# Performance work log

Measured on AMD Instinct MI355X. Metric: run time of the kernel, lower is better.

Reference implementation:

```python
import jax, jax.numpy as jnp
import numpy as np

B_SZ = 2
D_MODEL = 1024
H = 16
C = 8
BLK = 128
DK = 64
DV = 64
NCHUNK = 1024            # tokens per chunk (divisible by BLK)
T = C * (1 + NCHUNK)     # 8200: [g0, chunk0..., g1, chunk1..., ...]


def setup_inputs() -> dict:
    key = jax.random.key(0)
    k0, k1, k2, k3, k4 = jax.random.split(key, 5)
    s = 0.02
    x  = jax.random.normal(k0, (B_SZ, T, D_MODEL), dtype=jnp.float32)
    Wq = jax.random.normal(k1, (D_MODEL, H * DK), dtype=jnp.float32) * s
    Wk = jax.random.normal(k2, (D_MODEL, H * DK), dtype=jnp.float32) * s
    Wv = jax.random.normal(k3, (D_MODEL, H * DV), dtype=jnp.float32) * s
    Wo = jax.random.normal(k4, (H * DV, D_MODEL), dtype=jnp.float32) * s
    bo = jnp.zeros((D_MODEL,), dtype=jnp.float32)
    return {"x": x, "Wq": Wq, "Wk": Wk, "Wv": Wv, "Wo": Wo, "bo": bo}


def _local_sparse_3block(qf, kf, vf):
    # qf,kf: [BC, H, N, dk], vf: [BC, H, N, dv]; window = [left, current, right] blocks
    bc, h, n, dk = qf.shape
    dv = vf.shape[-1]
    nb = n // BLK
    q = qf.reshape(bc, h, nb, BLK, dk)
    k = kf.reshape(bc, h, nb, BLK, dk)
    v = vf.reshape(bc, h, nb, BLK, dv)
    zk = jnp.zeros((bc, h, 1, BLK, dk), qf.dtype)
    zv = jnp.zeros((bc, h, 1, BLK, dv), qf.dtype)
    kp = jnp.concatenate([zk, k, zk], axis=2)          # [bc,h,nb+2,B,dk]
    vp = jnp.concatenate([zv, v, zv], axis=2)
    k_win = jnp.concatenate([kp[:, :, 0:nb], kp[:, :, 1:nb + 1], kp[:, :, 2:nb + 2]], axis=3)  # [bc,h,nb,3B,dk]
    v_win = jnp.concatenate([vp[:, :, 0:nb], vp[:, :, 1:nb + 1], vp[:, :, 2:nb + 2]], axis=3)  # [bc,h,nb,3B,dv]
    scale = 1.0 / np.sqrt(dk).astype(np.float32)
    scores = jnp.einsum('bhnqd,bhnkd->bhnqk', q, k_win) * scale   # [bc,h,nb,B,3B]
    mask = np.zeros((nb, 3 * BLK), dtype=bool)
    mask[0, :BLK] = True           # first block: left padding invalid
    mask[-1, 2 * BLK:] = True      # last block: right padding invalid
    scores = jnp.where(jnp.asarray(mask)[None, None, :, None, :], -jnp.inf, scores)
    attn = jax.nn.softmax(scores, axis=-1)
    out = jnp.einsum('bhnqk,bhnkd->bhnqd', attn, v_win)
    return out.reshape(bc, h, n, dv)


def reference(x, Wq, Wk, Wv, Wo, bo):
    Bb, Tt, _ = x.shape
    q = (x @ Wq).reshape(Bb, Tt, H, DK).transpose(0, 2, 1, 3)  # [B,H,T,dk]
    k = (x @ Wk).reshape(Bb, Tt, H, DK).transpose(0, 2, 1, 3)
    v = (x @ Wv).reshape(Bb, Tt, H, DV).transpose(0, 2, 1, 3)
    stride = NCHUNK + 1
    g_idx = jnp.arange(C) * stride
    gq = q[:, :, g_idx]  # [B,H,C,dk]
    gk = k[:, :, g_idx]
    gv = v[:, :, g_idx]  # [B,H,C,dv]
    local_idx = ((g_idx + 1)[:, None] + jnp.arange(NCHUNK)[None, :]).reshape(-1)
    qx = q[:, :, local_idx].reshape(Bb, H, C, NCHUNK, DK)
    kx = k[:, :, local_idx].reshape(Bb, H, C, NCHUNK, DK)
    vx = v[:, :, local_idx].reshape(Bb, H, C, NCHUNK, DV)
    # local 3-block attention per chunk
    q_flat = qx.transpose(0, 2, 1, 3, 4).reshape(Bb * C, H, NCHUNK, DK)
    k_flat = kx.transpose(0, 2, 1, 3, 4).reshape(Bb * C, H, NCHUNK, DK)
    v_flat = vx.transpose(0, 2, 1, 3, 4).reshape(Bb * C, H, NCHUNK, DV)
    out_local = _local_sparse_3block(q_flat, k_flat, v_flat)
    out_local = out_local.reshape(Bb, C, H, NCHUNK, DV).transpose(0, 2, 1, 3, 4)  # [B,H,C,Nchunk,dv]
    # each local token additionally receives its chunk's global value directly
    out_chunks = out_local + gv[:, :, :, None, :]
    # global tokens attend over all globals + own chunk's locals (joint softmax, fp32)
    scale = 1.0 / np.sqrt(DK).astype(np.float32)
    scores_gg = jnp.einsum('bhcd,bhed->bhce', gq, gk) * scale      # [B,H,C,C]
    scores_gl = jnp.einsum('bhcd,bhcnd->bhcn', gq, kx) * scale     # [B,H,C,Nchunk]
    attn = jax.nn.softmax(jnp.concatenate([scores_gg, scores_gl], axis=-1), axis=-1)
    a_gg, a_gl = attn[..., :C], attn[..., C:]
    out_g = (jnp.einsum('bhce,bhed->bhcd', a_gg, gv)
             + jnp.einsum('bhcn,bhcnd->bhcd', a_gl, vx))           # [B,H,C,dv]
    out_inter = jnp.concatenate([out_g[:, :, :, None, :], out_chunks], axis=3)  # [B,H,C,1+Nchunk,dv]
    out = out_inter.reshape(Bb, H, Tt, DV).transpose(0, 2, 1, 3).reshape(Bb, Tt, H * DV)
    return out @ Wo + bo
```

## Files before the change

### kernel.cpp

```cpp
#include <hip/hip_runtime.h>
#include <hip/hip_bf16.h>

typedef __bf16 bf16x8 __attribute__((ext_vector_type(8)));
typedef float  f32x4  __attribute__((ext_vector_type(4)));
typedef unsigned short u16x8 __attribute__((ext_vector_type(8)));
typedef unsigned short u16x4 __attribute__((ext_vector_type(4)));
typedef unsigned u32x4 __attribute__((ext_vector_type(4)));
typedef unsigned long long u64x2 __attribute__((ext_vector_type(2)));

#define T_TOK   8200
#define M_TOK   16400
#define QKV_LD  3072
#define DM      1024

#define AS1CU const __attribute__((address_space(1))) unsigned int*
#define AS3U  __attribute__((address_space(3))) unsigned int*
#define GLDS16(g, s) __builtin_amdgcn_global_load_lds((AS1CU)(g), (AS3U)(s), 16, 0, 0)

__device__ __forceinline__ unsigned short f2bf(float f){
  __hip_bfloat16 h = __float2bfloat16(f);
  return *reinterpret_cast<unsigned short*>(&h);
}
__device__ __forceinline__ float bf2f(unsigned short u){
  union { unsigned u; float f; } x; x.u = ((unsigned)u) << 16;
  return x.f;
}

__global__ __launch_bounds__(256) void k_prep(const float* __restrict__ x, unsigned short* __restrict__ xb,
                                              const float* __restrict__ Wq, const float* __restrict__ Wk,
                                              const float* __restrict__ Wv, const float* __restrict__ Wo,
                                              unsigned short* __restrict__ wqkvt, unsigned short* __restrict__ wot){
  __shared__ float t[64][65];
  int bid = blockIdx.x, tid = threadIdx.x;
  if (bid < 2048){
    const long n4 = (long)M_TOK * 1024 / 4;
    long i = (long)bid * 256 + tid;
    const long stride = 2048L * 256;
    for (long e = i; e < n4; e += stride){
      float4 v = ((const float4*)x)[e];
      u16x4 o; o[0]=f2bf(v.x); o[1]=f2bf(v.y); o[2]=f2bf(v.z); o[3]=f2bf(v.w);
      ((u16x4*)xb)[e] = o;
    }
    return;
  }
  int bid2 = bid - 2048;
  int z = bid2 & 3; int rest = bid2 >> 2;
  int bx = rest & 15, by = rest >> 4;
  const float* W; unsigned short* Wt;
  if      (z == 0){ W = Wq; Wt = wqkvt; }
  else if (z == 1){ W = Wk; Wt = wqkvt + (size_t)1024*1024; }
  else if (z == 2){ W = Wv; Wt = wqkvt + (size_t)2048*1024; }
  else            { W = Wo; Wt = wot; }
  int tk0 = bx * 64, tn0 = by * 64;
#pragma unroll
  for (int i = 0; i < 4; i++){
    int ch = tid + i*256; int kr = ch >> 4, n4i = (ch & 15) * 4;
    float4 v = *(const float4*)(W + (size_t)(tk0+kr)*1024 + tn0 + n4i);
    t[kr][n4i+0]=v.x; t[kr][n4i+1]=v.y; t[kr][n4i+2]=v.z; t[kr][n4i+3]=v.w;
  }
  __syncthreads();
#pragma unroll
  for (int i = 0; i < 4; i++){
    int ch = tid + i*256; int nr = ch >> 4, k4 = (ch & 15) * 4;
    u16x4 o;
#pragma unroll
    for (int e = 0; e < 4; e++) o[e] = f2bf(t[k4+e][nr]);
    *(u16x4*)(Wt + (size_t)(tn0+nr)*1024 + tk0 + k4) = o;
  }
}

__global__ __launch_bounds__(256,2) void k_gemm(const unsigned short* __restrict__ A,
                                                const unsigned short* __restrict__ Bt,
                                                const float* __restrict__ bias,
                                                void* __restrict__ Cout,
                                                int M, int K, int ldc, int bf16out, int gn){
  __shared__ unsigned short As[128][64];
  __shared__ unsigned short Bs[128][64];
  int tid = threadIdx.x, l = tid & 63, w = tid >> 6;
  int li = l & 15, lh = l >> 4;
  int nwg = gridDim.x;
  int wg = (blockIdx.x & 7) * (nwg >> 3) + (blockIdx.x >> 3);
  int m0 = (wg / gn) * 128, n0 = (wg % gn) * 128;
  int wm = (w & 1) * 64, wn = (w >> 1) * 64;
  int lr = l >> 3, lc = l & 7;
  int lsw = li & 7;

  f32x4 acc[4][4];
#pragma unroll
  for (int a = 0; a < 4; a++)
#pragma unroll
    for (int b = 0; b < 4; b++) acc[a][b] = 0.f;

  for (int kt = 0; kt < K; kt += 64){
    __syncthreads();
#pragma unroll
    for (int i = 0; i < 4; i++){
      int r = w*32 + i*8 + lr;
      int colsw = (lc ^ (r & 7)) * 8;
      int rga = m0 + r; if (rga >= M) rga = M - 1;
      GLDS16(A  + (size_t)rga     *K + kt + colsw, &As[w*32 + i*8][0]);
      GLDS16(Bt + (size_t)(n0 + r)*K + kt + colsw, &Bs[w*32 + i*8][0]);
    }
    __syncthreads();
#pragma unroll
    for (int ks = 0; ks < 2; ks++){
      bf16x8 af[4], bfr[4];
#pragma unroll
      for (int mt = 0; mt < 4; mt++)
        af[mt] = *(const bf16x8*)&As[wm + mt*16 + li][((ks*4 + lh) ^ lsw) * 8];
#pragma unroll
      for (int nt = 0; nt < 4; nt++)
        bfr[nt] = *(const bf16x8*)&Bs[wn + nt*16 + li][((ks*4 + lh) ^ lsw) * 8];
#pragma unroll
      for (int mt = 0; mt < 4; mt++)
#pragma unroll
        for (int nt = 0; nt < 4; nt++)
          acc[mt][nt] = __builtin_amdgcn_mfma_f32_16x16x32_bf16(af[mt], bfr[nt], acc[mt][nt], 0, 0, 0);
    }
  }
#pragma unroll
  for (int mt = 0; mt < 4; mt++)
#pragma unroll
    for (int nt = 0; nt < 4; nt++)
#pragma unroll
      for (int r = 0; r < 4; r++){
        int row = m0 + wm + mt*16 + lh*4 + r;
        int col = n0 + wn + nt*16 + li;
        if (row < M){
          float v = acc[mt][nt][r] + (bias ? bias[col] : 0.f);
          if (bf16out) ((unsigned short*)Cout)[(size_t)row*ldc + col] = f2bf(v);
          else         ((float*)Cout)[(size_t)row*ldc + col] = v;
        }
      }
}

__global__ __launch_bounds__(256,3) void k_local(const unsigned short* __restrict__ qkv,
                                                 unsigned short* __restrict__ att){
  __shared__ unsigned short Ks[128][64];
  __shared__ unsigned short Vt[64][136];

  int tid = threadIdx.x;

  if (blockIdx.x >= 2048){
    float* sc   = (float*)&Ks[0][0];
    float* red  = sc + 1032;
    float* gq_s = red + 256;
    int gid = blockIdx.x - 2048;
    int c = gid & 7, h = (gid >> 3) & 15, b = gid >> 7;
    size_t bT = (size_t)b * T_TOK;
    size_t grow = bT + (size_t)c*1025;
    if (tid < 64) gq_s[tid] = bf2f(qkv[grow*QKV_LD + h*64 + tid]);
    __syncthreads();
    float lmax = -3e38f;
    for (int idx = tid; idx < 1032; idx += 256){
      size_t krow = (idx < 8) ? (bT + (size_t)idx*1025) : (bT + (size_t)c*1025 + 1 + (idx - 8));
      const unsigned short* kp = qkv + krow*QKV_LD + 1024 + h*64;
      float s = 0.f;
#pragma unroll
      for (int d0 = 0; d0 < 64; d0 += 8){
        u16x8 kv = *(const u16x8*)(kp + d0);
#pragma unroll
        for (int e = 0; e < 8; e++) s += gq_s[d0+e] * bf2f(kv[e]);
      }
      s *= 0.125f;
      sc[idx] = s;
      lmax = fmaxf(lmax, s);
    }
    red[tid] = lmax; __syncthreads();
    for (int st = 128; st > 0; st >>= 1){ if (tid < st) red[tid] = fmaxf(red[tid], red[tid+st]); __syncthreads(); }
    float m = red[0]; __syncthreads();
    float lsum = 0.f;
    for (int idx = tid; idx < 1032; idx += 256){
      float p = __expf(sc[idx] - m); sc[idx] = p; lsum += p;
    }
    red[tid] = lsum; __syncthreads();
    for (int st = 128; st > 0; st >>= 1){ if (tid < st) red[tid] += red[tid+st]; __syncthreads(); }
    float denom = red[0]; __syncthreads();
    int d = tid & 63, part = tid >> 6;
    float acc = 0.f;
    for (int idx = part; idx < 1032; idx += 4){
      size_t krow = (idx < 8) ? (bT + (size_t)idx*1025) : (bT + (size_t)c*1025 + 1 + (idx - 8));
      acc += sc[idx] * bf2f(qkv[krow*QKV_LD + 2048 + h*64 + d]);
    }
    red[tid] = acc; __syncthreads();
    if (tid < 64){
      float o = (red[tid] + red[tid+64] + red[tid+128] + red[tid+192]) / denom;
      att[grow*DM + h*64 + tid] = f2bf(o);
    }
    return;
  }

  int l = tid & 63, w = tid >> 6;
  int li = l & 15, lh = l >> 4;
  int lr = l >> 3, lc = l & 7;
  int lsw = li & 7;
  int wg = (blockIdx.x & 7) * 256 + (blockIdx.x >> 3);
  int blk = wg & 7, c = (wg >> 3) & 7, h = (wg >> 6) & 15, b = wg >> 10;
  size_t bT = (size_t)b * T_TOK;
  int tokq0 = c*1025 + 1 + blk*128;

  bf16x8 aq[2][2];
#pragma unroll
  for (int tr = 0; tr < 2; tr++)
#pragma unroll
    for (int ks = 0; ks < 2; ks++)
      aq[tr][ks] = *(const bf16x8*)(qkv + (bT + tokq0 + w*32 + tr*16 + li)*QKV_LD + h*64 + ks*32 + lh*8);

  float psum[2] = {0.f, 0.f};
  f32x4 oacc[2][4];
#pragma unroll
  for (int tr = 0; tr < 2; tr++)
#pragma unroll
    for (int ct = 0; ct < 4; ct++) oacc[tr][ct] = 0.f;

  for (int kb = blk-1; kb <= blk+1; ++kb){
    if ((unsigned)kb > 7u) continue;
    int tokk0 = c*1025 + 1 + kb*128;

    u16x8 vlo[2], vhi[2];
#pragma unroll
    for (int i = 0; i < 2; i++){
      int gv = 4*i + w;
      const unsigned short* vp = qkv + (bT + tokk0 + 2*l)*QKV_LD + 2048 + h*64 + gv*8;
      vlo[i] = *(const u16x8*)vp;
      vhi[i] = *(const u16x8*)(vp + QKV_LD);
    }
    __syncthreads();
#pragma unroll
    for (int i = 0; i < 4; i++){
      int r = w*32 + i*8 + lr;
      int colk = (lc ^ (r & 7)) * 8;
      GLDS16(qkv + (bT + tokk0 + r)*QKV_LD + 1024 + h*64 + colk, &Ks[w*32 + i*8][0]);
    }
#pragma unroll
    for (int i = 0; i < 2; i++)
#pragma unroll
      for (int e = 0; e < 8; e++){
        unsigned pk = (unsigned)vlo[i][e] | ((unsigned)vhi[i][e] << 16);
        *(unsigned*)&Vt[(4*i + w)*8 + e][2*l] = pk;
      }
    __syncthreads();

#pragma unroll
    for (int tr = 0; tr < 2; tr++){
      f32x4 s[8];
#pragma unroll
      for (int ct = 0; ct < 8; ct++) s[ct] = 0.f;
#pragma unroll
      for (int ct = 0; ct < 8; ct++)
#pragma unroll
        for (int ks = 0; ks < 2; ks++){
          bf16x8 kf = *(const bf16x8*)&Ks[ct*16 + li][((ks*4 + lh) ^ lsw) * 8];
          s[ct] = __builtin_amdgcn_mfma_f32_16x16x32_bf16(kf, aq[tr][ks], s[ct], 0, 0, 0);
        }
#pragma unroll
      for (int ks = 0; ks < 4; ks++){
        float q0 = __expf(s[2*ks  ][0] * 0.125f);
        float q1 = __expf(s[2*ks  ][1] * 0.125f);
        float q2 = __expf(s[2*ks  ][2] * 0.125f);
        float q3 = __expf(s[2*ks  ][3] * 0.125f);
        float q4 = __expf(s[2*ks+1][0] * 0.125f);
        float q5 = __expf(s[2*ks+1][1] * 0.125f);
        float q6 = __expf(s[2*ks+1][2] * 0.125f);
        float q7 = __expf(s[2*ks+1][3] * 0.125f);
        psum[tr] += ((q0 + q1) + (q2 + q3)) + ((q4 + q5) + (q6 + q7));
        u32x4 frv;
        frv.x = (unsigned)f2bf(q0) | ((unsigned)f2bf(q1) << 16);
        frv.y = (unsigned)f2bf(q2) | ((unsigned)f2bf(q3) << 16);
        frv.z = (unsigned)f2bf(q4) | ((unsigned)f2bf(q5) << 16);
        frv.w = (unsigned)f2bf(q6) | ((unsigned)f2bf(q7) << 16);
        bf16x8 pa = __builtin_bit_cast(bf16x8, frv);
        int base = ks*16 + 2*lh;
#pragma unroll
        for (int ct = 0; ct < 4; ct++){
          const unsigned* vrow = (const unsigned*)&Vt[ct*16 + li][0];
          u64x2 vfv;
          vfv.x = *(const unsigned long long*)(vrow + base);
          vfv.y = *(const unsigned long long*)(vrow + base + 8);
          bf16x8 vf = __builtin_bit_cast(bf16x8, vfv);
          oacc[tr][ct] = __builtin_amdgcn_mfma_f32_16x16x32_bf16(pa, vf, oacc[tr][ct], 0, 0, 0);
        }
      }
    }
  }

#pragma unroll
  for (int tr = 0; tr < 2; tr++){
    psum[tr] += __shfl_xor(psum[tr], 16, 64);
    psum[tr] += __shfl_xor(psum[tr], 32, 64);
  }
  float ps[2][4];
#pragma unroll
  for (int tr = 0; tr < 2; tr++)
#pragma unroll
    for (int r = 0; r < 4; r++)
      ps[tr][r] = __shfl(psum[tr], lh*4 + r, 64);
  float gvv[4];
#pragma unroll
  for (int ct = 0; ct < 4; ct++)
    gvv[ct] = bf2f(qkv[(bT + c*1025)*QKV_LD + 2048 + h*64 + ct*16 + li]);
#pragma unroll
  for (int tr = 0; tr < 2; tr++)
#pragma unroll
    for (int ct = 0; ct < 4; ct++)
#pragma unroll
      for (int r = 0; r < 4; r++){
        int row = w*32 + tr*16 + lh*4 + r;
        float v = oacc[tr][ct][r] / ps[tr][r] + gvv[ct];
        att[(bT + tokq0 + row)*DM + h*64 + ct*16 + li] = f2bf(v);
      }
}

extern "C" void kernel_launch(void* const* d_in, const int* in_sizes, int n_in,
                              void* d_out, int out_size, void* d_ws, size_t ws_size,
                              hipStream_t stream) {
  const float* x  = (const float*)d_in[0];
  const float* Wq = (const float*)d_in[1];
  const float* Wk = (const float*)d_in[2];
  const float* Wv = (const float*)d_in[3];
  const float* Wo = (const float*)d_in[4];
  const float* bo = (const float*)d_in[5];
  float* out = (float*)d_out;

  unsigned short* xb    = (unsigned short*)d_ws;
  unsigned short* wqkvt = xb    + (size_t)M_TOK * 1024;
  unsigned short* wot   = wqkvt + (size_t)3072 * 1024;
  unsigned short* qkv   = wot   + (size_t)1024 * 1024;
  unsigned short* att   = qkv   + (size_t)M_TOK * QKV_LD;

  k_prep<<<3072, 256, 0, stream>>>(x, xb, Wq, Wk, Wv, Wo, wqkvt, wot);
  k_gemm<<<dim3(129*24), 256, 0, stream>>>(xb, wqkvt, (const float*)nullptr, (void*)qkv,
                                           M_TOK, 1024, QKV_LD, 1, 24);
  k_local<<<2304, 256, 0, stream>>>(qkv, att);
  k_gemm<<<dim3(129*8), 256, 0, stream>>>(att, wot, bo, (void*)out,
                                          M_TOK, 1024, DM, 0, 8);
}
```

Baseline: 339.9 us.

## Schedule global-token blocks first and interleave two row tiles in local attention

Moves the 256 global-token blocks to the front of the grid so their long serial reductions start early instead of forming a tail after the local blocks. In the local attention loop, both 16-row query tiles are now computed together, so each K fragment and V fragment read from LDS feeds two MFMAs. This halves LDS fragment reads and gives the scheduler independent MFMA chains to interleave. In exchange it holds 16 score accumulators at once, which raises register pressure and could reduce occupancy under launch_bounds(256,3).

```diff
diff --git a/kernel.cpp b/kernel.cpp
--- a/kernel.cpp
+++ b/kernel.cpp
@@ -141,11 +141,11 @@
 
   int tid = threadIdx.x;
 
-  if (blockIdx.x >= 2048){
+  if (blockIdx.x < 256){
     float* sc   = (float*)&Ks[0][0];
     float* red  = sc + 1032;
     float* gq_s = red + 256;
-    int gid = blockIdx.x - 2048;
+    int gid = blockIdx.x;
     int c = gid & 7, h = (gid >> 3) & 15, b = gid >> 7;
     size_t bT = (size_t)b * T_TOK;
     size_t grow = bT + (size_t)c*1025;
@@ -194,7 +194,8 @@
   int li = l & 15, lh = l >> 4;
   int lr = l >> 3, lc = l & 7;
   int lsw = li & 7;
-  int wg = (blockIdx.x & 7) * 256 + (blockIdx.x >> 3);
+  int wg0 = blockIdx.x - 256;
+  int wg = (wg0 & 7) * 256 + (wg0 >> 3);
   int blk = wg & 7, c = (wg >> 3) & 7, h = (wg >> 6) & 15, b = wg >> 10;
   size_t bT = (size_t)b * T_TOK;
   int tokq0 = c*1025 + 1 + blk*128;
@@ -241,45 +242,51 @@
       }
     __syncthreads();
 
-#pragma unroll
-    for (int tr = 0; tr < 2; tr++){
-      f32x4 s[8];
-#pragma unroll
-      for (int ct = 0; ct < 8; ct++) s[ct] = 0.f;
-#pragma unroll
-      for (int ct = 0; ct < 8; ct++)
-#pragma unroll
-        for (int ks = 0; ks < 2; ks++){
-          bf16x8 kf = *(const bf16x8*)&Ks[ct*16 + li][((ks*4 + lh) ^ lsw) * 8];
-          s[ct] = __builtin_amdgcn_mfma_f32_16x16x32_bf16(kf, aq[tr][ks], s[ct], 0, 0, 0);
-        }
-#pragma unroll
-      for (int ks = 0; ks < 4; ks++){
-        float q0 = __expf(s[2*ks  ][0] * 0.125f);
-        float q1 = __expf(s[2*ks  ][1] * 0.125f);
-        float q2 = __expf(s[2*ks  ][2] * 0.125f);
-        float q3 = __expf(s[2*ks  ][3] * 0.125f);
-        float q4 = __expf(s[2*ks+1][0] * 0.125f);
-        float q5 = __expf(s[2*ks+1][1] * 0.125f);
-        float q6 = __expf(s[2*ks+1][2] * 0.125f);
-        float q7 = __expf(s[2*ks+1][3] * 0.125f);
+    f32x4 s2[2][8];
+#pragma unroll
+    for (int tr = 0; tr < 2; tr++)
+#pragma unroll
+      for (int ct = 0; ct < 8; ct++) s2[tr][ct] = 0.f;
+#pragma unroll
+    for (int ct = 0; ct < 8; ct++)
+#pragma unroll
+      for (int ks = 0; ks < 2; ks++){
+        bf16x8 kf = *(const bf16x8*)&Ks[ct*16 + li][((ks*4 + lh) ^ lsw) * 8];
+        s2[0][ct] = __builtin_amdgcn_mfma_f32_16x16x32_bf16(kf, aq[0][ks], s2[0][ct], 0, 0, 0);
+        s2[1][ct] = __builtin_amdgcn_mfma_f32_16x16x32_bf16(kf, aq[1][ks], s2[1][ct], 0, 0, 0);
+      }
+
+#pragma unroll
+    for (int ks = 0; ks < 4; ks++){
+      bf16x8 pa[2];
+#pragma unroll
+      for (int tr = 0; tr < 2; tr++){
+        float q0 = __expf(s2[tr][2*ks  ][0] * 0.125f);
+        float q1 = __expf(s2[tr][2*ks  ][1] * 0.125f);
+        float q2 = __expf(s2[tr][2*ks  ][2] * 0.125f);
+        float q3 = __expf(s2[tr][2*ks  ][3] * 0.125f);
+        float q4 = __expf(s2[tr][2*ks+1][0] * 0.125f);
+        float q5 = __expf(s2[tr][2*ks+1][1] * 0.125f);
+        float q6 = __expf(s2[tr][2*ks+1][2] * 0.125f);
+        float q7 = __expf(s2[tr][2*ks+1][3] * 0.125f);
         psum[tr] += ((q0 + q1) + (q2 + q3)) + ((q4 + q5) + (q6 + q7));
         u32x4 frv;
         frv.x = (unsigned)f2bf(q0) | ((unsigned)f2bf(q1) << 16);
         frv.y = (unsigned)f2bf(q2) | ((unsigned)f2bf(q3) << 16);
         frv.z = (unsigned)f2bf(q4) | ((unsigned)f2bf(q5) << 16);
         frv.w = (unsigned)f2bf(q6) | ((unsigned)f2bf(q7) << 16);
-        bf16x8 pa = __builtin_bit_cast(bf16x8, frv);
-        int base = ks*16 + 2*lh;
-#pragma unroll
-        for (int ct = 0; ct < 4; ct++){
-          const unsigned* vrow = (const unsigned*)&Vt[ct*16 + li][0];
-          u64x2 vfv;
-          vfv.x = *(const unsigned long long*)(vrow + base);
-          vfv.y = *(const unsigned long long*)(vrow + base + 8);
-          bf16x8 vf = __builtin_bit_cast(bf16x8, vfv);
-          oacc[tr][ct] = __builtin_amdgcn_mfma_f32_16x16x32_bf16(pa, vf, oacc[tr][ct], 0, 0, 0);
-        }
+        pa[tr] = __builtin_bit_cast(bf16x8, frv);
+      }
+      int base = ks*16 + 2*lh;
+#pragma unroll
+      for (int ct = 0; ct < 4; ct++){
+        const unsigned* vrow = (const unsigned*)&Vt[ct*16 + li][0];
+        u64x2 vfv;
+        vfv.x = *(const unsigned long long*)(vrow + base);
+        vfv.y = *(const unsigned long long*)(vrow + base + 8);
+        bf16x8 vf = __builtin_bit_cast(bf16x8, vfv);
+        oacc[0][ct] = __builtin_amdgcn_mfma_f32_16x16x32_bf16(pa[0], vf, oacc[0][ct], 0, 0, 0);
+        oacc[1][ct] = __builtin_amdgcn_mfma_f32_16x16x32_bf16(pa[1], vf, oacc[1][ct], 0, 0, 0);
       }
     }
   }
```

Result: faster. 296.9 us, median of 2 (-12.6%).
